# Kernel tuning notes

Measured on AMD Instinct MI355X. Metric: run time of the kernel, lower is better.

Reference implementation:

```python
import jax, jax.numpy as jnp
import numpy as np
from jax import lax

N = 16384
M = 16384
C = 64
NUM_CORR = 2048
EPS = 1e-08


def setup_inputs() -> dict:
    key = jax.random.key(0)
    k1, k2, k3, k4 = jax.random.split(key, 4)
    src_points = jax.random.normal(k1, (N, 3), dtype=jnp.float32)
    tgt_points = jax.random.normal(k2, (M, 3), dtype=jnp.float32)
    # features are L2-normalized descriptors in the original pipeline
    src_feats = jax.random.normal(k3, (N, C), dtype=jnp.float32)
    tgt_feats = jax.random.normal(k4, (M, C), dtype=jnp.float32)
    src_feats = src_feats / jnp.linalg.norm(src_feats, axis=-1, keepdims=True)
    tgt_feats = tgt_feats / jnp.linalg.norm(tgt_feats, axis=-1, keepdims=True)
    return {"src_points": src_points, "tgt_points": tgt_points,
            "src_feats": src_feats, "tgt_feats": tgt_feats}


def _match_one_side(q_points, s_points, q_feats, s_feats):
    # brute-force feature kNN (k=2) by squared euclidean distance
    # dist2[n,m] = ||q_n||^2 - 2 q_n.s_m + ||s_m||^2
    dist2 = (jnp.sum(q_feats * q_feats, axis=-1, keepdims=True)
             - 2.0 * (q_feats @ s_feats.T)
             + jnp.sum(s_feats * s_feats, axis=-1)[None, :])  # [N, M]
    _, knn_indices = lax.top_k(-dist2, 2)  # [N, 2]
    knn_feats = s_feats[knn_indices]  # [N, 2, C]
    knn_similarities = 1.0 - jnp.einsum('nkc,nc->nk', knn_feats, q_feats)  # [N, 2]
    # Lowe's ratio test weight
    weights = 1.0 - knn_similarities[:, 0] / (knn_similarities[:, 1] + EPS)  # [N]
    _, q_corr_indices = lax.top_k(weights, NUM_CORR)  # [K]
    s_corr_indices = knn_indices[q_corr_indices, 0]  # [K]
    return (q_points[q_corr_indices], s_points[s_corr_indices],
            q_feats[q_corr_indices], s_feats[s_corr_indices],
            weights[q_corr_indices])


def reference(src_points, tgt_points, src_feats, tgt_feats):
    (s1_pts, t1_pts, s1_feats, t1_feats, w1) = _match_one_side(
        src_points, tgt_points, src_feats, tgt_feats)
    (t2_pts, s2_pts, t2_feats, s2_feats, w2) = _match_one_side(
        tgt_points, src_points, tgt_feats, src_feats)
    src_corr_points = jnp.concatenate([s1_pts, s2_pts], axis=0)
    tgt_corr_points = jnp.concatenate([t1_pts, t2_pts], axis=0)
    src_corr_feats = jnp.concatenate([s1_feats, s2_feats], axis=0)
    tgt_corr_feats = jnp.concatenate([t1_feats, t2_feats], axis=0)
    corr_weights = jnp.concatenate([w1, w2], axis=0)
    return (src_corr_points, tgt_corr_points, src_corr_feats,
            tgt_corr_feats, corr_weights)
```

## Files before the change

### kernel.cpp

```cpp
#include <hip/hip_runtime.h>

#define NPTS 16384
#define CF 64
#define KCORR 2048
#define TCAND 64


__device__ __forceinline__ float dot_avx2(const float* __restrict__ a,
                                          const float* __restrict__ b) {
#pragma clang fp contract(off)
    float v0 = 0.f, v1 = 0.f, v2 = 0.f, v3 = 0.f;
    float v4 = 0.f, v5 = 0.f, v6 = 0.f, v7 = 0.f;
    #pragma unroll
    for (int i = 0; i < CF; i += 8) {
        v0 = fmaf(a[i + 0], b[i + 0], v0);
        v1 = fmaf(a[i + 1], b[i + 1], v1);
        v2 = fmaf(a[i + 2], b[i + 2], v2);
        v3 = fmaf(a[i + 3], b[i + 3], v3);
        v4 = fmaf(a[i + 4], b[i + 4], v4);
        v5 = fmaf(a[i + 5], b[i + 5], v5);
        v6 = fmaf(a[i + 6], b[i + 6], v6);
        v7 = fmaf(a[i + 7], b[i + 7], v7);
    }
    float u0 = v0 + v4, u1 = v1 + v5, u2 = v2 + v6, u3 = v3 + v7;
    float t0 = u0 + u2, t1 = u1 + u3;
    return t0 + t1;
}

__device__ __forceinline__ float row_sumsq(const float* __restrict__ x) {
#pragma clang fp contract(off)
    float r[8];
    #pragma unroll
    for (int j = 0; j < 8; ++j) r[j] = x[j] * x[j];
    #pragma unroll
    for (int i = 8; i < 64; i += 8) {
        #pragma unroll
        for (int j = 0; j < 8; ++j) { float p = x[i + j] * x[i + j]; r[j] = r[j] + p; }
    }
    return ((r[0] + r[1]) + (r[2] + r[3])) + ((r[4] + r[5]) + (r[6] + r[7]));
}

__device__ __forceinline__ float dot_fma(const float* __restrict__ a,
                                         const float* __restrict__ b) {
    float acc = 0.0f;
    #pragma unroll
    for (int c = 0; c < CF; ++c) acc = fmaf(a[c], b[c], acc);
    return acc;
}

__global__ __launch_bounds__(256) void prep_kernel(
    const float* __restrict__ src_feats, const float* __restrict__ tgt_feats,
    float* __restrict__ qq_src, float* __restrict__ qq_tgt)
{
    int t = blockIdx.x * 256 + threadIdx.x;
    if (t >= 2 * NPTS) return;
    const float* f = (t < NPTS) ? src_feats : tgt_feats;
    float*      qq = (t < NPTS) ? qq_src    : qq_tgt;
    int n = (t < NPTS) ? t : t - NPTS;
    float x[CF];
    #pragma unroll
    for (int c = 0; c < CF; c += 4) {
        float4 v = *(const float4*)(f + (size_t)n * CF + c);
        x[c] = v.x; x[c+1] = v.y; x[c+2] = v.z; x[c+3] = v.w;
    }
    qq[n] = row_sumsq(x);
}

__global__ __launch_bounds__(256) void top2_kernel(
    const float* __restrict__ src_feats, const float* __restrict__ tgt_feats,
    const float* __restrict__ qq_src, const float* __restrict__ qq_tgt,
    float* __restrict__ pd0, float* __restrict__ pd1,
    int* __restrict__ pi0, int* __restrict__ pi1,
    int nch, int chsz)
{
    const int side = blockIdx.z;
    const int ch   = blockIdx.y;
    const int tid  = threadIdx.x;
    const int n    = blockIdx.x * 256 + tid;

    const float* qf = (side == 0) ? src_feats : tgt_feats;
    const float* sf = (side == 0) ? tgt_feats : src_feats;
    const float* qq = (side == 0) ? qq_src    : qq_tgt;
    const float* ss = (side == 0) ? qq_tgt    : qq_src;

    __shared__ float sd[TCAND][CF];
    __shared__ float sss[TCAND];

    float qd[CF];
    #pragma unroll
    for (int c = 0; c < CF; c += 4) {
        float4 v = *(const float4*)(qf + (size_t)n * CF + c);
        qd[c] = v.x; qd[c+1] = v.y; qd[c+2] = v.z; qd[c+3] = v.w;
    }
    const float qqn = qq[n];

    float d0 = 3.4e38f, d1 = 3.4e38f;
    int i0 = 0, i1 = 0;

    const int m0 = ch * chsz;
    float* sflat = &sd[0][0];
    for (int t0 = 0; t0 < chsz; t0 += TCAND) {
        __syncthreads();
        const float4* g4 = (const float4*)(sf + (size_t)(m0 + t0) * CF);
        #pragma unroll
        for (int k = 0; k < 4; ++k) {
            int idx = k * 256 + tid;
            float4 v = g4[idx];
            sflat[idx*4+0] = v.x; sflat[idx*4+1] = v.y;
            sflat[idx*4+2] = v.z; sflat[idx*4+3] = v.w;
        }
        if (tid < TCAND) sss[tid] = ss[m0 + t0 + tid];
        __syncthreads();

        #pragma unroll 2
        for (int mm = 0; mm < TCAND; ++mm) {
            const float* s = sd[mm];
            float dot = dot_fma(qd, s);
            float d2;
            {
#pragma clang fp contract(off)
                float twod = 2.0f * dot;
                float t1v  = qqn - twod;
                d2 = t1v + sss[mm];
            }
            int m = m0 + t0 + mm;
            if (d2 < d1) {
                if (d2 < d0) { d1 = d0; i1 = i0; d0 = d2; i0 = m; }
                else         { d1 = d2; i1 = m; }
            }
        }
    }
    size_t slot = ((size_t)side * nch + ch) * NPTS + n;
    pd0[slot] = d0; pd1[slot] = d1;
    pi0[slot] = i0; pi1[slot] = i1;
}

__global__ __launch_bounds__(256) void merge_kernel(
    const float* __restrict__ src_feats, const float* __restrict__ tgt_feats,
    const float* __restrict__ pd0, const float* __restrict__ pd1,
    const int* __restrict__ pi0, const int* __restrict__ pi1,
    int nch,
    float* __restrict__ wgt, int* __restrict__ bidx)
{
    int t = blockIdx.x * blockDim.x + threadIdx.x;
    if (t >= 2 * NPTS) return;
    int side = t >> 14, n = t & (NPTS - 1);

    float d0 = 3.4e38f, d1 = 3.4e38f;
    int i0 = 0, i1 = 0;
    for (int ch = 0; ch < nch; ++ch) {
        size_t slot = ((size_t)side * nch + ch) * NPTS + n;
        float cd0 = pd0[slot], cd1 = pd1[slot];
        int   ci0 = pi0[slot], ci1 = pi1[slot];
        if (cd0 < d1) {
            if (cd0 < d0) { d1 = d0; i1 = i0; d0 = cd0; i0 = ci0; }
            else          { d1 = cd0; i1 = ci0; }
        }
        if (cd1 < d1) {
            if (cd1 < d0) { d1 = d0; i1 = i0; d0 = cd1; i0 = ci1; }
            else          { d1 = cd1; i1 = ci1; }
        }
    }
    if (i0 < 0) i0 = 0;
    if (i1 < 0) i1 = 0;

    const float* qf = (side == 0) ? src_feats : tgt_feats;
    const float* sf = (side == 0) ? tgt_feats : src_feats;

    float q[CF];
    #pragma unroll
    for (int c = 0; c < CF; c += 4) {
        float4 v = *(const float4*)(qf + (size_t)n * CF + c);
        q[c] = v.x; q[c+1] = v.y; q[c+2] = v.z; q[c+3] = v.w;
    }

    float dotA = dot_avx2(sf + (size_t)i0 * CF, q);
    float dotB = dot_avx2(sf + (size_t)i1 * CF, q);

    float w;
    {
#pragma clang fp contract(off)
        float sim0 = 1.0f - dotA;
        float sim1 = 1.0f - dotB;
        float den  = sim1 + 1e-8f;
        w = 1.0f - sim0 / den;
    }
    wgt[t]  = w;
    bidx[t] = i0;
}

__global__ __launch_bounds__(256) void rank_gather_kernel(
    const float* __restrict__ wgt, const int* __restrict__ bidx,
    const float* __restrict__ src_points, const float* __restrict__ tgt_points,
    const float* __restrict__ src_feats,  const float* __restrict__ tgt_feats,
    float* __restrict__ out)
{
    const int side = blockIdx.y;
    const int n = blockIdx.x * 256 + threadIdx.x;
    const float* w = wgt + (size_t)side * NPTS;
    const float wn = w[n];

    __shared__ float tile[4096];
    int cnt = 0;
    for (int t0 = 0; t0 < NPTS; t0 += 4096) {
        __syncthreads();
        for (int j = threadIdx.x; j < 4096; j += 256) tile[j] = w[t0 + j];
        __syncthreads();
        #pragma unroll 8
        for (int j = 0; j < 4096; ++j) {
            float wj = tile[j];
            int jj = t0 + j;
            cnt += (wj > wn) || (wj == wn && jj < n);
        }
    }

    if (cnt < KCORR) {
        int r = side * KCORR + cnt;
        int sidx = bidx[(size_t)side * NPTS + n];
        if (sidx < 0) sidx = 0;
        int src_row = (side == 0) ? n : sidx;
        int tgt_row = (side == 0) ? sidx : n;

        float* out_srcP = out;
        float* out_tgtP = out + 2 * KCORR * 3;
        float* out_srcF = out + 4 * KCORR * 3;
        float* out_tgtF = out_srcF + 2 * KCORR * CF;
        float* out_w    = out_tgtF + 2 * KCORR * CF;

        #pragma unroll
        for (int k = 0; k < 3; ++k) {
            out_srcP[(size_t)r * 3 + k] = src_points[(size_t)src_row * 3 + k];
            out_tgtP[(size_t)r * 3 + k] = tgt_points[(size_t)tgt_row * 3 + k];
        }
        const float4* sfr = (const float4*)(src_feats + (size_t)src_row * CF);
        const float4* tfr = (const float4*)(tgt_feats + (size_t)tgt_row * CF);
        float4* so = (float4*)(out_srcF + (size_t)r * CF);
        float4* to = (float4*)(out_tgtF + (size_t)r * CF);
        #pragma unroll
        for (int c = 0; c < CF / 4; ++c) { so[c] = sfr[c]; to[c] = tfr[c]; }
        out_w[r] = wn;
    }
}

extern "C" void kernel_launch(void* const* d_in, const int* in_sizes, int n_in,
                              void* d_out, int out_size, void* d_ws, size_t ws_size,
                              hipStream_t stream)
{
    const float* src_points = (const float*)d_in[0];
    const float* tgt_points = (const float*)d_in[1];
    const float* src_feats  = (const float*)d_in[2];
    const float* tgt_feats  = (const float*)d_in[3];
    float* out = (float*)d_out;
    (void)in_sizes; (void)n_in; (void)out_size;

    auto rup = [](size_t b) { return (b + 255) & ~(size_t)255; };
    size_t base = rup(sizeof(float) * NPTS) * 2
                + rup(sizeof(float) * 2 * NPTS)
                + rup(sizeof(int) * 2 * NPTS);
    size_t per_chunk = rup(sizeof(float) * 2 * NPTS) * 2
                     + rup(sizeof(int) * 2 * NPTS) * 2;
    int nch = 16;
    while (nch > 1 && base + (size_t)nch * per_chunk > ws_size) nch >>= 1;
    int chsz = NPTS / nch;
    size_t nslots = (size_t)2 * nch * NPTS;

    char* ws = (char*)d_ws;
    size_t off = 0;
    auto alloc = [&](size_t bytes) -> void* {
        void* p = ws + off;
        off += (bytes + 255) & ~(size_t)255;
        return p;
    };
    float* qq_src = (float*)alloc(sizeof(float) * NPTS);
    float* qq_tgt = (float*)alloc(sizeof(float) * NPTS);
    float* wgt    = (float*)alloc(sizeof(float) * 2 * NPTS);
    int*   bidx   = (int*)alloc(sizeof(int) * 2 * NPTS);
    float* pd0    = (float*)alloc(sizeof(float) * nslots);
    float* pd1    = (float*)alloc(sizeof(float) * nslots);
    int*   pi0    = (int*)alloc(sizeof(int) * nslots);
    int*   pi1    = (int*)alloc(sizeof(int) * nslots);

    prep_kernel<<<(2 * NPTS + 255) / 256, 256, 0, stream>>>(
        src_feats, tgt_feats, qq_src, qq_tgt);

    top2_kernel<<<dim3(NPTS / 256, nch, 2), 256, 0, stream>>>(
        src_feats, tgt_feats, qq_src, qq_tgt,
        pd0, pd1, pi0, pi1, nch, chsz);

    merge_kernel<<<(2 * NPTS + 255) / 256, 256, 0, stream>>>(
        src_feats, tgt_feats, pd0, pd1, pi0, pi1, nch, wgt, bidx);

    rank_gather_kernel<<<dim3(NPTS / 256, 2), 256, 0, stream>>>(
        wgt, bidx, src_points, tgt_points, src_feats, tgt_feats, out);
}
```

Baseline: 1.498 ms.

## Register-block kNN distance tile as 8x8 outer-product SGEMM with fused top-2

Replaces the one-query-per-thread candidate scan with a 128x128 block tile where each thread computes an 8x8 outer-product accumulator from transposed shared-memory Q and candidate tiles. It fuses the per-thread top-2 selection and an intra-block top-2 merge, removing candidate chunking and the multi-chunk merge in the merge kernel. The intent is to raise FMA-to-LDS-load ratio; the trade-off is a grid of only 256 blocks with heavier register use and no load/compute overlap.

```diff
diff --git a/kernel.cpp b/kernel.cpp
--- a/kernel.cpp
+++ b/kernel.cpp
@@ -3,8 +3,8 @@
 #define NPTS 16384
 #define CF 64
 #define KCORR 2048
-#define TCAND 64
-
+#define TQ 128
+#define TC 128
 
 __device__ __forceinline__ float dot_avx2(const float* __restrict__ a,
                                           const float* __restrict__ b) {
@@ -40,14 +40,6 @@
     return ((r[0] + r[1]) + (r[2] + r[3])) + ((r[4] + r[5]) + (r[6] + r[7]));
 }
 
-__device__ __forceinline__ float dot_fma(const float* __restrict__ a,
-                                         const float* __restrict__ b) {
-    float acc = 0.0f;
-    #pragma unroll
-    for (int c = 0; c < CF; ++c) acc = fmaf(a[c], b[c], acc);
-    return acc;
-}
-
 __global__ __launch_bounds__(256) void prep_kernel(
     const float* __restrict__ src_feats, const float* __restrict__ tgt_feats,
     float* __restrict__ qq_src, float* __restrict__ qq_tgt)
@@ -70,99 +62,156 @@
     const float* __restrict__ src_feats, const float* __restrict__ tgt_feats,
     const float* __restrict__ qq_src, const float* __restrict__ qq_tgt,
     float* __restrict__ pd0, float* __restrict__ pd1,
-    int* __restrict__ pi0, int* __restrict__ pi1,
-    int nch, int chsz)
-{
-    const int side = blockIdx.z;
-    const int ch   = blockIdx.y;
+    int* __restrict__ pi0, int* __restrict__ pi1)
+{
+    const int side = blockIdx.y;
+    const int qb   = blockIdx.x;
     const int tid  = threadIdx.x;
-    const int n    = blockIdx.x * 256 + tid;
-
-    const float* qf = (side == 0) ? src_feats : tgt_feats;
-    const float* sf = (side == 0) ? tgt_feats : src_feats;
-    const float* qq = (side == 0) ? qq_src    : qq_tgt;
-    const float* ss = (side == 0) ? qq_tgt    : qq_src;
-
-    __shared__ float sd[TCAND][CF];
-    __shared__ float sss[TCAND];
-
-    float qd[CF];
-    #pragma unroll
-    for (int c = 0; c < CF; c += 4) {
-        float4 v = *(const float4*)(qf + (size_t)n * CF + c);
-        qd[c] = v.x; qd[c+1] = v.y; qd[c+2] = v.z; qd[c+3] = v.w;
-    }
-    const float qqn = qq[n];
-
-    float d0 = 3.4e38f, d1 = 3.4e38f;
-    int i0 = 0, i1 = 0;
-
-    const int m0 = ch * chsz;
-    float* sflat = &sd[0][0];
-    for (int t0 = 0; t0 < chsz; t0 += TCAND) {
+    const int ty   = tid >> 4;
+    const int tx   = tid & 15;
+
+    const float* qf  = (side == 0) ? src_feats : tgt_feats;
+    const float* sf  = (side == 0) ? tgt_feats : src_feats;
+    const float* qqp = (side == 0) ? qq_src    : qq_tgt;
+    const float* ssp = (side == 0) ? qq_tgt    : qq_src;
+
+    __shared__ float Qs[CF][TQ];
+    __shared__ float Cs[CF][TC];
+
+    #pragma unroll
+    for (int i = 0; i < 8; ++i) {
+        int flat = i * 256 + tid;
+        int row  = flat >> 4;
+        int k4   = flat & 15;
+        float4 v = *(const float4*)(qf + (size_t)(qb * TQ + row) * CF + k4 * 4);
+        Qs[k4*4+0][row] = v.x; Qs[k4*4+1][row] = v.y;
+        Qs[k4*4+2][row] = v.z; Qs[k4*4+3][row] = v.w;
+    }
+
+    float qqv[8];
+    #pragma unroll
+    for (int i = 0; i < 8; ++i) qqv[i] = qqp[qb * TQ + ty * 8 + i];
+
+    float rd0[8], rd1[8];
+    int   ri0[8], ri1[8];
+    #pragma unroll
+    for (int i = 0; i < 8; ++i) {
+        rd0[i] = 3.4e38f; rd1[i] = 3.4e38f;
+        ri0[i] = 0x7fffffff; ri1[i] = 0x7fffffff;
+    }
+
+    for (int tile = 0; tile < NPTS / TC; ++tile) {
         __syncthreads();
-        const float4* g4 = (const float4*)(sf + (size_t)(m0 + t0) * CF);
-        #pragma unroll
-        for (int k = 0; k < 4; ++k) {
-            int idx = k * 256 + tid;
-            float4 v = g4[idx];
-            sflat[idx*4+0] = v.x; sflat[idx*4+1] = v.y;
-            sflat[idx*4+2] = v.z; sflat[idx*4+3] = v.w;
-        }
-        if (tid < TCAND) sss[tid] = ss[m0 + t0 + tid];
+        #pragma unroll
+        for (int i = 0; i < 8; ++i) {
+            int flat = i * 256 + tid;
+            int row  = flat >> 4;
+            int k4   = flat & 15;
+            float4 v = *(const float4*)(sf + (size_t)(tile * TC + row) * CF + k4 * 4);
+            Cs[k4*4+0][row] = v.x; Cs[k4*4+1][row] = v.y;
+            Cs[k4*4+2][row] = v.z; Cs[k4*4+3][row] = v.w;
+        }
         __syncthreads();
 
-        #pragma unroll 2
-        for (int mm = 0; mm < TCAND; ++mm) {
-            const float* s = sd[mm];
-            float dot = dot_fma(qd, s);
-            float d2;
-            {
+        float ssv[8];
+        #pragma unroll
+        for (int i = 0; i < 8; ++i) ssv[i] = ssp[tile * TC + tx * 8 + i];
+
+        float acc[8][8];
+        #pragma unroll
+        for (int a = 0; a < 8; ++a)
+            #pragma unroll
+            for (int b = 0; b < 8; ++b) acc[a][b] = 0.0f;
+
+        #pragma unroll 4
+        for (int k = 0; k < CF; ++k) {
+            float4 a0 = *(const float4*)&Qs[k][ty * 8];
+            float4 a1 = *(const float4*)&Qs[k][ty * 8 + 4];
+            float4 b0 = *(const float4*)&Cs[k][tx * 8];
+            float4 b1 = *(const float4*)&Cs[k][tx * 8 + 4];
+            float qv[8] = {a0.x, a0.y, a0.z, a0.w, a1.x, a1.y, a1.z, a1.w};
+            float cv[8] = {b0.x, b0.y, b0.z, b0.w, b1.x, b1.y, b1.z, b1.w};
+            #pragma unroll
+            for (int qi = 0; qi < 8; ++qi)
+                #pragma unroll
+                for (int ci = 0; ci < 8; ++ci)
+                    acc[qi][ci] = fmaf(qv[qi], cv[ci], acc[qi][ci]);
+        }
+
+        #pragma unroll
+        for (int qi = 0; qi < 8; ++qi) {
+            float qqn = qqv[qi];
+            #pragma unroll
+            for (int ci = 0; ci < 8; ++ci) {
+                float d2;
+                {
 #pragma clang fp contract(off)
-                float twod = 2.0f * dot;
-                float t1v  = qqn - twod;
-                d2 = t1v + sss[mm];
+                    float twod = 2.0f * acc[qi][ci];
+                    float t1v  = qqn - twod;
+                    d2 = t1v + ssv[ci];
+                }
+                int m = tile * TC + tx * 8 + ci;
+                if (d2 < rd1[qi]) {
+                    if (d2 < rd0[qi]) { rd1[qi] = rd0[qi]; ri1[qi] = ri0[qi];
+                                        rd0[qi] = d2;      ri0[qi] = m; }
+                    else              { rd1[qi] = d2;      ri1[qi] = m; }
+                }
             }
-            int m = m0 + t0 + mm;
-            if (d2 < d1) {
-                if (d2 < d0) { d1 = d0; i1 = i0; d0 = d2; i0 = m; }
-                else         { d1 = d2; i1 = m; }
+        }
+    }
+
+    __syncthreads();
+    float (*md0)[TQ] = (float (*)[TQ])&Qs[0][0];
+    float (*md1)[TQ] = (float (*)[TQ])&Qs[16][0];
+    int   (*mi0)[TQ] = (int   (*)[TQ])&Qs[32][0];
+    int   (*mi1)[TQ] = (int   (*)[TQ])&Qs[48][0];
+    #pragma unroll
+    for (int qi = 0; qi < 8; ++qi) {
+        int q = ty * 8 + qi;
+        md0[tx][q] = rd0[qi]; md1[tx][q] = rd1[qi];
+        mi0[tx][q] = ri0[qi]; mi1[tx][q] = ri1[qi];
+    }
+    __syncthreads();
+
+    if (tid < TQ) {
+        int q = tid;
+        float d0 = 3.4e38f, d1 = 3.4e38f;
+        int   i0 = 0x7fffffff, i1 = 0x7fffffff;
+        for (int t = 0; t < 16; ++t) {
+            float cd0 = md0[t][q], cd1 = md1[t][q];
+            int   ci0 = mi0[t][q], ci1 = mi1[t][q];
+            if (cd0 < d1 || (cd0 == d1 && ci0 < i1)) {
+                if (cd0 < d0 || (cd0 == d0 && ci0 < i0)) {
+                    d1 = d0; i1 = i0; d0 = cd0; i0 = ci0;
+                } else { d1 = cd0; i1 = ci0; }
             }
-        }
-    }
-    size_t slot = ((size_t)side * nch + ch) * NPTS + n;
-    pd0[slot] = d0; pd1[slot] = d1;
-    pi0[slot] = i0; pi1[slot] = i1;
+            if (cd1 < d1 || (cd1 == d1 && ci1 < i1)) {
+                if (cd1 < d0 || (cd1 == d0 && ci1 < i0)) {
+                    d1 = d0; i1 = i0; d0 = cd1; i0 = ci1;
+                } else { d1 = cd1; i1 = ci1; }
+            }
+        }
+        size_t slot = (size_t)side * NPTS + qb * TQ + q;
+        pd0[slot] = d0; pd1[slot] = d1;
+        pi0[slot] = i0; pi1[slot] = i1;
+    }
 }
 
 __global__ __launch_bounds__(256) void merge_kernel(
     const float* __restrict__ src_feats, const float* __restrict__ tgt_feats,
     const float* __restrict__ pd0, const float* __restrict__ pd1,
     const int* __restrict__ pi0, const int* __restrict__ pi1,
-    int nch,
     float* __restrict__ wgt, int* __restrict__ bidx)
 {
     int t = blockIdx.x * blockDim.x + threadIdx.x;
     if (t >= 2 * NPTS) return;
     int side = t >> 14, n = t & (NPTS - 1);
 
-    float d0 = 3.4e38f, d1 = 3.4e38f;
-    int i0 = 0, i1 = 0;
-    for (int ch = 0; ch < nch; ++ch) {
-        size_t slot = ((size_t)side * nch + ch) * NPTS + n;
-        float cd0 = pd0[slot], cd1 = pd1[slot];
-        int   ci0 = pi0[slot], ci1 = pi1[slot];
-        if (cd0 < d1) {
-            if (cd0 < d0) { d1 = d0; i1 = i0; d0 = cd0; i0 = ci0; }
-            else          { d1 = cd0; i1 = ci0; }
-        }
-        if (cd1 < d1) {
-            if (cd1 < d0) { d1 = d0; i1 = i0; d0 = cd1; i0 = ci1; }
-            else          { d1 = cd1; i1 = ci1; }
-        }
-    }
-    if (i0 < 0) i0 = 0;
-    if (i1 < 0) i1 = 0;
+    size_t slot = (size_t)side * NPTS + n;
+    int i0 = pi0[slot], i1 = pi1[slot];
+    (void)pd0; (void)pd1;
+    if (i0 < 0 || i0 >= NPTS) i0 = 0;
+    if (i1 < 0 || i1 >= NPTS) i1 = 0;
 
     const float* qf = (side == 0) ? src_feats : tgt_feats;
     const float* sf = (side == 0) ? tgt_feats : src_feats;
@@ -251,18 +300,7 @@
     const float* src_feats  = (const float*)d_in[2];
     const float* tgt_feats  = (const float*)d_in[3];
     float* out = (float*)d_out;
-    (void)in_sizes; (void)n_in; (void)out_size;
-
-    auto rup = [](size_t b) { return (b + 255) & ~(size_t)255; };
-    size_t base = rup(sizeof(float) * NPTS) * 2
-                + rup(sizeof(float) * 2 * NPTS)
-                + rup(sizeof(int) * 2 * NPTS);
-    size_t per_chunk = rup(sizeof(float) * 2 * NPTS) * 2
-                     + rup(sizeof(int) * 2 * NPTS) * 2;
-    int nch = 16;
-    while (nch > 1 && base + (size_t)nch * per_chunk > ws_size) nch >>= 1;
-    int chsz = NPTS / nch;
-    size_t nslots = (size_t)2 * nch * NPTS;
+    (void)in_sizes; (void)n_in; (void)out_size; (void)ws_size;
 
     char* ws = (char*)d_ws;
     size_t off = 0;
@@ -275,20 +313,19 @@
     float* qq_tgt = (float*)alloc(sizeof(float) * NPTS);
     float* wgt    = (float*)alloc(sizeof(float) * 2 * NPTS);
     int*   bidx   = (int*)alloc(sizeof(int) * 2 * NPTS);
-    float* pd0    = (float*)alloc(sizeof(float) * nslots);
-    float* pd1    = (float*)alloc(sizeof(float) * nslots);
-    int*   pi0    = (int*)alloc(sizeof(int) * nslots);
-    int*   pi1    = (int*)alloc(sizeof(int) * nslots);
+    float* pd0    = (float*)alloc(sizeof(float) * 2 * NPTS);
+    float* pd1    = (float*)alloc(sizeof(float) * 2 * NPTS);
+    int*   pi0    = (int*)alloc(sizeof(int) * 2 * NPTS);
+    int*   pi1    = (int*)alloc(sizeof(int) * 2 * NPTS);
 
     prep_kernel<<<(2 * NPTS + 255) / 256, 256, 0, stream>>>(
         src_feats, tgt_feats, qq_src, qq_tgt);
 
-    top2_kernel<<<dim3(NPTS / 256, nch, 2), 256, 0, stream>>>(
-        src_feats, tgt_feats, qq_src, qq_tgt,
-        pd0, pd1, pi0, pi1, nch, chsz);
+    top2_kernel<<<dim3(NPTS / TQ, 2), 256, 0, stream>>>(
+        src_feats, tgt_feats, qq_src, qq_tgt, pd0, pd1, pi0, pi1);
 
     merge_kernel<<<(2 * NPTS + 255) / 256, 256, 0, stream>>>(
-        src_feats, tgt_feats, pd0, pd1, pi0, pi1, nch, wgt, bidx);
+        src_feats, tgt_feats, pd0, pd1, pi0, pi1, wgt, bidx);
 
     rank_gather_kernel<<<dim3(NPTS / 256, 2), 256, 0, stream>>>(
         wgt, bidx, src_points, tgt_points, src_feats, tgt_feats, out);
```

Result: slower. 1.944 ms (+29.8%).

## Screen kNN candidates with bf16 MFMA, then refine survivors in exact fp32

Applied to the files above, without the earlier changes.

Replaces the scalar fp32 brute-force top-2 search with a two-pass scheme. Pass one converts features to bf16 and uses MFMA 16x16x32 to compute approximate distances, keeping a per-query threshold (second-best plus a fixed margin). Pass two recomputes the bf16 distances and runs an exact fp32 dot product only for candidates under that threshold, so the final top-2 keeps reference precision. Chunked partial results and the merge loop go away, but the distance matrix is computed twice. The fixed 0.03 margin assumes bf16 error stays below it for unit-norm features, and candidate rows are read straight from global memory without LDS staging.

```diff
diff --git a/kernel.cpp b/kernel.cpp
--- a/kernel.cpp
+++ b/kernel.cpp
@@ -1,10 +1,20 @@
 #include <hip/hip_runtime.h>
+
+typedef unsigned short ushort_t;
 
 #define NPTS 16384
 #define CF 64
 #define KCORR 2048
-#define TCAND 64
-
+
+typedef __attribute__((ext_vector_type(8))) short bf16x8;
+typedef __attribute__((ext_vector_type(4))) float f32x4;
+
+__device__ __forceinline__ ushort_t f2bf(float f) {
+    union { float f; unsigned int i; } x; x.f = f;
+    unsigned int u = x.i;
+    u += 0x7FFFu + ((u >> 16) & 1);
+    return (ushort_t)(u >> 16);
+}
 
 __device__ __forceinline__ float dot_avx2(const float* __restrict__ a,
                                           const float* __restrict__ b) {
@@ -48,6 +58,16 @@
     return acc;
 }
 
+__global__ __launch_bounds__(256) void conv_kernel(
+    const float* __restrict__ src_feats, const float* __restrict__ tgt_feats,
+    ushort_t* __restrict__ sfb, ushort_t* __restrict__ tfb)
+{
+    int i = blockIdx.x * 256 + threadIdx.x;
+    if (i >= NPTS * CF) return;
+    sfb[i] = f2bf(src_feats[i]);
+    tfb[i] = f2bf(tgt_feats[i]);
+}
+
 __global__ __launch_bounds__(256) void prep_kernel(
     const float* __restrict__ src_feats, const float* __restrict__ tgt_feats,
     float* __restrict__ qq_src, float* __restrict__ qq_tgt)
@@ -66,103 +86,159 @@
     qq[n] = row_sumsq(x);
 }
 
-__global__ __launch_bounds__(256) void top2_kernel(
+__global__ __launch_bounds__(256) void screen_kernel(
+    const ushort_t* __restrict__ sfb, const ushort_t* __restrict__ tfb,
+    const float* __restrict__ qq_src, const float* __restrict__ qq_tgt,
+    float* __restrict__ T)
+{
+    const int side = blockIdx.y;
+    const int qb   = blockIdx.x;
+    const int w    = threadIdx.x >> 6;
+    const int lane = threadIdx.x & 63;
+
+    const ushort_t* qfb = (side == 0) ? sfb : tfb;
+    const ushort_t* cfb = (side == 0) ? tfb : sfb;
+    const float*    qq  = (side == 0) ? qq_src : qq_tgt;
+    const float*    ss  = (side == 0) ? qq_tgt : qq_src;
+
+    const int qrow = qb * 64 + w * 16 + (lane & 15);
+    const int kofs = (lane >> 4) * 8;
+
+    bf16x8 bq0 = *(const bf16x8*)(qfb + (size_t)qrow * CF + kofs);
+    bf16x8 bq1 = *(const bf16x8*)(qfb + (size_t)qrow * CF + 32 + kofs);
+    const float qqn = qq[qrow];
+
+    float m1 = 3.4e38f, m2 = 3.4e38f;
+
+    #pragma unroll 2
+    for (int tile = 0; tile < NPTS / 16; ++tile) {
+        const int cbase = tile * 16;
+        const ushort_t* cr = cfb + (size_t)(cbase + (lane & 15)) * CF + kofs;
+        bf16x8 a0 = *(const bf16x8*)(cr);
+        bf16x8 a1 = *(const bf16x8*)(cr + 32);
+        f32x4 acc = {0.f, 0.f, 0.f, 0.f};
+        acc = __builtin_amdgcn_mfma_f32_16x16x32_bf16(a0, bq0, acc, 0, 0, 0);
+        acc = __builtin_amdgcn_mfma_f32_16x16x32_bf16(a1, bq1, acc, 0, 0, 0);
+        const int rb = cbase + (lane >> 4) * 4;
+        #pragma unroll
+        for (int j = 0; j < 4; ++j) {
+            float d2 = qqn - 2.0f * acc[j] + ss[rb + j];
+            if (d2 < m2) { if (d2 < m1) { m2 = m1; m1 = d2; } else m2 = d2; }
+        }
+    }
+
+    #pragma unroll
+    for (int off = 16; off <= 32; off <<= 1) {
+        float o1 = __shfl_xor(m1, off, 64);
+        float o2 = __shfl_xor(m2, off, 64);
+        float n1 = fminf(m1, o1);
+        float n2 = fminf(fmaxf(m1, o1), fminf(m2, o2));
+        m1 = n1; m2 = n2;
+    }
+    if (lane < 16) T[(size_t)side * NPTS + qrow] = m2 + 0.03f;
+}
+
+__global__ __launch_bounds__(256) void refine_kernel(
+    const ushort_t* __restrict__ sfb, const ushort_t* __restrict__ tfb,
     const float* __restrict__ src_feats, const float* __restrict__ tgt_feats,
     const float* __restrict__ qq_src, const float* __restrict__ qq_tgt,
+    const float* __restrict__ T,
     float* __restrict__ pd0, float* __restrict__ pd1,
-    int* __restrict__ pi0, int* __restrict__ pi1,
-    int nch, int chsz)
-{
-    const int side = blockIdx.z;
-    const int ch   = blockIdx.y;
-    const int tid  = threadIdx.x;
-    const int n    = blockIdx.x * 256 + tid;
-
-    const float* qf = (side == 0) ? src_feats : tgt_feats;
-    const float* sf = (side == 0) ? tgt_feats : src_feats;
-    const float* qq = (side == 0) ? qq_src    : qq_tgt;
-    const float* ss = (side == 0) ? qq_tgt    : qq_src;
-
-    __shared__ float sd[TCAND][CF];
-    __shared__ float sss[TCAND];
-
-    float qd[CF];
-    #pragma unroll
-    for (int c = 0; c < CF; c += 4) {
-        float4 v = *(const float4*)(qf + (size_t)n * CF + c);
-        qd[c] = v.x; qd[c+1] = v.y; qd[c+2] = v.z; qd[c+3] = v.w;
-    }
-    const float qqn = qq[n];
-
-    float d0 = 3.4e38f, d1 = 3.4e38f;
-    int i0 = 0, i1 = 0;
-
-    const int m0 = ch * chsz;
-    float* sflat = &sd[0][0];
-    for (int t0 = 0; t0 < chsz; t0 += TCAND) {
-        __syncthreads();
-        const float4* g4 = (const float4*)(sf + (size_t)(m0 + t0) * CF);
-        #pragma unroll
-        for (int k = 0; k < 4; ++k) {
-            int idx = k * 256 + tid;
-            float4 v = g4[idx];
-            sflat[idx*4+0] = v.x; sflat[idx*4+1] = v.y;
-            sflat[idx*4+2] = v.z; sflat[idx*4+3] = v.w;
-        }
-        if (tid < TCAND) sss[tid] = ss[m0 + t0 + tid];
-        __syncthreads();
-
-        #pragma unroll 2
-        for (int mm = 0; mm < TCAND; ++mm) {
-            const float* s = sd[mm];
-            float dot = dot_fma(qd, s);
-            float d2;
-            {
+    int* __restrict__ pi0, int* __restrict__ pi1)
+{
+    const int side = blockIdx.y;
+    const int qb   = blockIdx.x;
+    const int w    = threadIdx.x >> 6;
+    const int lane = threadIdx.x & 63;
+
+    const ushort_t* qfb = (side == 0) ? sfb : tfb;
+    const ushort_t* cfb = (side == 0) ? tfb : sfb;
+    const float*    qf  = (side == 0) ? src_feats : tgt_feats;
+    const float*    cf  = (side == 0) ? tgt_feats : src_feats;
+    const float*    qq  = (side == 0) ? qq_src : qq_tgt;
+    const float*    ss  = (side == 0) ? qq_tgt : qq_src;
+
+    const int qrow = qb * 64 + w * 16 + (lane & 15);
+    const int kofs = (lane >> 4) * 8;
+
+    bf16x8 bq0 = *(const bf16x8*)(qfb + (size_t)qrow * CF + kofs);
+    bf16x8 bq1 = *(const bf16x8*)(qfb + (size_t)qrow * CF + 32 + kofs);
+    const float qqn = qq[qrow];
+    const float Tq  = T[(size_t)side * NPTS + qrow];
+    const float* qp = qf + (size_t)qrow * CF;
+
+    float rd0 = 3.4e38f, rd1 = 3.4e38f;
+    int   ri0 = 0x7fffffff, ri1 = 0x7fffffff;
+
+    #pragma unroll 2
+    for (int tile = 0; tile < NPTS / 16; ++tile) {
+        const int cbase = tile * 16;
+        const ushort_t* cr = cfb + (size_t)(cbase + (lane & 15)) * CF + kofs;
+        bf16x8 a0 = *(const bf16x8*)(cr);
+        bf16x8 a1 = *(const bf16x8*)(cr + 32);
+        f32x4 acc = {0.f, 0.f, 0.f, 0.f};
+        acc = __builtin_amdgcn_mfma_f32_16x16x32_bf16(a0, bq0, acc, 0, 0, 0);
+        acc = __builtin_amdgcn_mfma_f32_16x16x32_bf16(a1, bq1, acc, 0, 0, 0);
+        const int rb = cbase + (lane >> 4) * 4;
+        #pragma unroll
+        for (int j = 0; j < 4; ++j) {
+            float d2b = qqn - 2.0f * acc[j] + ss[rb + j];
+            if (d2b <= Tq) {
+                int cand = rb + j;
+                float dote = dot_fma(qp, cf + (size_t)cand * CF);
+                float d2e;
+                {
 #pragma clang fp contract(off)
-                float twod = 2.0f * dot;
-                float t1v  = qqn - twod;
-                d2 = t1v + sss[mm];
-            }
-            int m = m0 + t0 + mm;
-            if (d2 < d1) {
-                if (d2 < d0) { d1 = d0; i1 = i0; d0 = d2; i0 = m; }
-                else         { d1 = d2; i1 = m; }
+                    float twod = 2.0f * dote;
+                    float t1v  = qqn - twod;
+                    d2e = t1v + ss[cand];
+                }
+                if (d2e < rd1 || (d2e == rd1 && cand < ri1)) {
+                    if (d2e < rd0 || (d2e == rd0 && cand < ri0)) {
+                        rd1 = rd0; ri1 = ri0; rd0 = d2e; ri0 = cand;
+                    } else { rd1 = d2e; ri1 = cand; }
+                }
             }
         }
     }
-    size_t slot = ((size_t)side * nch + ch) * NPTS + n;
-    pd0[slot] = d0; pd1[slot] = d1;
-    pi0[slot] = i0; pi1[slot] = i1;
+
+    #pragma unroll
+    for (int off = 16; off <= 32; off <<= 1) {
+        float od0 = __shfl_xor(rd0, off, 64);
+        float od1 = __shfl_xor(rd1, off, 64);
+        int   oi0 = __shfl_xor(ri0, off, 64);
+        int   oi1 = __shfl_xor(ri1, off, 64);
+        bool aw = (rd0 < od0) || (rd0 == od0 && ri0 < oi0);
+        float w1d = aw ? rd0 : od0;  int w1i = aw ? ri0 : oi0;
+        float l1d = aw ? od0 : rd0;  int l1i = aw ? oi0 : ri0;
+        float s1d = aw ? rd1 : od1;  int s1i = aw ? ri1 : oi1;
+        bool bw = (s1d < l1d) || (s1d == l1d && s1i < l1i);
+        float w2d = bw ? s1d : l1d;  int w2i = bw ? s1i : l1i;
+        rd0 = w1d; ri0 = w1i; rd1 = w2d; ri1 = w2i;
+    }
+
+    if (lane < 16) {
+        size_t slot = (size_t)side * NPTS + qrow;
+        pd0[slot] = rd0; pd1[slot] = rd1;
+        pi0[slot] = ri0; pi1[slot] = ri1;
+    }
 }
 
 __global__ __launch_bounds__(256) void merge_kernel(
     const float* __restrict__ src_feats, const float* __restrict__ tgt_feats,
     const float* __restrict__ pd0, const float* __restrict__ pd1,
     const int* __restrict__ pi0, const int* __restrict__ pi1,
-    int nch,
     float* __restrict__ wgt, int* __restrict__ bidx)
 {
     int t = blockIdx.x * blockDim.x + threadIdx.x;
     if (t >= 2 * NPTS) return;
     int side = t >> 14, n = t & (NPTS - 1);
 
-    float d0 = 3.4e38f, d1 = 3.4e38f;
-    int i0 = 0, i1 = 0;
-    for (int ch = 0; ch < nch; ++ch) {
-        size_t slot = ((size_t)side * nch + ch) * NPTS + n;
-        float cd0 = pd0[slot], cd1 = pd1[slot];
-        int   ci0 = pi0[slot], ci1 = pi1[slot];
-        if (cd0 < d1) {
-            if (cd0 < d0) { d1 = d0; i1 = i0; d0 = cd0; i0 = ci0; }
-            else          { d1 = cd0; i1 = ci0; }
-        }
-        if (cd1 < d1) {
-            if (cd1 < d0) { d1 = d0; i1 = i0; d0 = cd1; i0 = ci1; }
-            else          { d1 = cd1; i1 = ci1; }
-        }
-    }
-    if (i0 < 0) i0 = 0;
-    if (i1 < 0) i1 = 0;
+    size_t slot = (size_t)side * NPTS + n;
+    int i0 = pi0[slot], i1 = pi1[slot];
+    (void)pd0; (void)pd1;
+    if (i0 < 0 || i0 >= NPTS) i0 = 0;
+    if (i1 < 0 || i1 >= NPTS) i1 = 0;
 
     const float* qf = (side == 0) ? src_feats : tgt_feats;
     const float* sf = (side == 0) ? tgt_feats : src_feats;
@@ -251,18 +327,7 @@
     const float* src_feats  = (const float*)d_in[2];
     const float* tgt_feats  = (const float*)d_in[3];
     float* out = (float*)d_out;
-    (void)in_sizes; (void)n_in; (void)out_size;
-
-    auto rup = [](size_t b) { return (b + 255) & ~(size_t)255; };
-    size_t base = rup(sizeof(float) * NPTS) * 2
-                + rup(sizeof(float) * 2 * NPTS)
-                + rup(sizeof(int) * 2 * NPTS);
-    size_t per_chunk = rup(sizeof(float) * 2 * NPTS) * 2
-                     + rup(sizeof(int) * 2 * NPTS) * 2;
-    int nch = 16;
-    while (nch > 1 && base + (size_t)nch * per_chunk > ws_size) nch >>= 1;
-    int chsz = NPTS / nch;
-    size_t nslots = (size_t)2 * nch * NPTS;
+    (void)in_sizes; (void)n_in; (void)out_size; (void)ws_size;
 
     char* ws = (char*)d_ws;
     size_t off = 0;
@@ -271,24 +336,33 @@
         off += (bytes + 255) & ~(size_t)255;
         return p;
     };
+    ushort_t* sfb = (ushort_t*)alloc(sizeof(ushort_t) * (size_t)NPTS * CF);
+    ushort_t* tfb = (ushort_t*)alloc(sizeof(ushort_t) * (size_t)NPTS * CF);
     float* qq_src = (float*)alloc(sizeof(float) * NPTS);
     float* qq_tgt = (float*)alloc(sizeof(float) * NPTS);
+    float* T      = (float*)alloc(sizeof(float) * 2 * NPTS);
     float* wgt    = (float*)alloc(sizeof(float) * 2 * NPTS);
     int*   bidx   = (int*)alloc(sizeof(int) * 2 * NPTS);
-    float* pd0    = (float*)alloc(sizeof(float) * nslots);
-    float* pd1    = (float*)alloc(sizeof(float) * nslots);
-    int*   pi0    = (int*)alloc(sizeof(int) * nslots);
-    int*   pi1    = (int*)alloc(sizeof(int) * nslots);
+    float* pd0    = (float*)alloc(sizeof(float) * 2 * NPTS);
+    float* pd1    = (float*)alloc(sizeof(float) * 2 * NPTS);
+    int*   pi0    = (int*)alloc(sizeof(int) * 2 * NPTS);
+    int*   pi1    = (int*)alloc(sizeof(int) * 2 * NPTS);
+
+    conv_kernel<<<(NPTS * CF + 255) / 256, 256, 0, stream>>>(
+        src_feats, tgt_feats, sfb, tfb);
 
     prep_kernel<<<(2 * NPTS + 255) / 256, 256, 0, stream>>>(
         src_feats, tgt_feats, qq_src, qq_tgt);
 
-    top2_kernel<<<dim3(NPTS / 256, nch, 2), 256, 0, stream>>>(
-        src_feats, tgt_feats, qq_src, qq_tgt,
-        pd0, pd1, pi0, pi1, nch, chsz);
+    screen_kernel<<<dim3(NPTS / 64, 2), 256, 0, stream>>>(
+        sfb, tfb, qq_src, qq_tgt, T);
+
+    refine_kernel<<<dim3(NPTS / 64, 2), 256, 0, stream>>>(
+        sfb, tfb, src_feats, tgt_feats, qq_src, qq_tgt, T,
+        pd0, pd1, pi0, pi1);
 
     merge_kernel<<<(2 * NPTS + 255) / 256, 256, 0, stream>>>(
-        src_feats, tgt_feats, pd0, pd1, pi0, pi1, nch, wgt, bidx);
+        src_feats, tgt_feats, pd0, pd1, pi0, pi1, wgt, bidx);
 
     rank_gather_kernel<<<dim3(NPTS / 256, 2), 256, 0, stream>>>(
         wgt, bidx, src_points, tgt_points, src_feats, tgt_feats, out);
```

New measurement: 1.792 ms. 19.6% more time.
